# Kernel tuning notes

Measured on AMD Instinct MI355X. Metric: run time of the kernel, lower is better.

Reference implementation:

```python
import jax, jax.numpy as jnp
import numpy as np

N_NODES = 8192
N_UND = 65536      # undirected pairs placed
N_DIR = 131072     # extra directed edges placed


def _build_graph():
    rng = np.random.default_rng(0)
    A = np.zeros((N_NODES, N_NODES), np.float32)
    # undirected pairs (i<j), both directions set
    ii = rng.integers(0, N_NODES, 4 * N_UND)
    jj = rng.integers(0, N_NODES, 4 * N_UND)
    m = ii < jj
    iu, ju = ii[m][:N_UND], jj[m][:N_UND]
    A[iu, ju] = 1.0
    A[ju, iu] = 1.0
    # extra directed edges
    di = rng.integers(0, N_NODES, 2 * N_DIR)
    dj = rng.integers(0, N_NODES, 2 * N_DIR)
    m2 = di != dj
    A[di[m2][:N_DIR], dj[m2][:N_DIR]] = 1.0
    # dense_to_sparse: row, col of nonzeros
    row, col = np.nonzero(A)
    edge_index = np.stack([row, col]).astype(np.int32)
    # undirected mask: A==1 & A.T==1, upper triangle
    und = np.triu((A == 1.0) & (A.T == 1.0))
    u, v = np.nonzero(und)
    undirected_edges = np.stack([u, v], axis=1).astype(np.int32)
    return A, edge_index, undirected_edges


def setup_inputs() -> dict:
    key = jax.random.key(0)
    ks = jax.random.split(key, 4)
    A, edge_index, undirected_edges = _build_graph()
    N = N_NODES
    return {
        "adjacency": jnp.asarray(A),
        "W1": jax.random.normal(ks[0], (N, 16), jnp.float32) * 0.05,
        "b1": jnp.zeros((16,), jnp.float32),
        "W2": jax.random.normal(ks[1], (16, 8), jnp.float32) * 0.25,
        "b2": jnp.zeros((8,), jnp.float32),
        "Wfc": jax.random.normal(ks[2], (16, 1), jnp.float32) * 0.25,
        "bfc": jnp.zeros((1,), jnp.float32),
        "edge_index": jnp.asarray(edge_index),
        "undirected_edges": jnp.asarray(undirected_edges),
    }


def reference(adjacency, W1, b1, W2, b2, Wfc, bfc, edge_index, undirected_edges):
    N = adjacency.shape[0]
    src, dst = edge_index[0], edge_index[1]
    E = src.shape[0]
    # GCN normalization with self-loops (PyG gcn_norm): deg over target nodes
    deg = jax.ops.segment_sum(jnp.ones((E,), adjacency.dtype), dst,
                              num_segments=N) + 1.0
    dinv = jax.lax.rsqrt(deg)                       # deg >= 1, no inf
    norm = dinv[src] * dinv[dst]                    # [E]
    self_w = (dinv * dinv)[:, None]                 # self-loop coeff [N,1]

    def conv(h):  # h: [N, F] -> normalized scatter-add aggregation
        msg = norm[:, None] * h[src]                # [E, F]
        return jax.ops.segment_sum(msg, dst, num_segments=N) + self_w * h

    # node_features = eye(N), so eye(N) @ W1 == W1
    x = jax.nn.relu(conv(W1) + b1)                  # [N, 16]
    x = jax.nn.relu(conv(x @ W2) + b2)              # [N, 8]

    u, v = undirected_edges[:, 0], undirected_edges[:, 1]
    ef = jnp.concatenate([x[u], x[v]], axis=1)      # [U, 16]
    orient = jax.nn.sigmoid(ef @ Wfc + bfc)[:, 0]   # [U]

    out = adjacency.at[u, v].set(orient).at[v, u].set(1.0 - orient)
    return out
```

## Files before the change

kernel.cpp:

```cpp
#include <hip/hip_runtime.h>
#include <math.h>

#define F1 16
#define F2 8

typedef float f32x4 __attribute__((ext_vector_type(4)));

__global__ void k_zero4(f32x4* __restrict__ p, long n4) {
    long i = (long)blockIdx.x * blockDim.x + threadIdx.x;
    long stride = (long)gridDim.x * blockDim.x;
    f32x4 z = {0.0f, 0.0f, 0.0f, 0.0f};
    for (; i < n4; i += stride) {
        __builtin_nontemporal_store(z, &p[i]);
    }
}

__global__ void k_edges0(const int* __restrict__ src, const int* __restrict__ dst,
                         float* __restrict__ out, float* __restrict__ deg,
                         int E, int N) {
    int e = blockIdx.x * blockDim.x + threadIdx.x;
    if (e < E) {
        int s = src[e], d = dst[e];
        out[(long)s * N + d] = 1.0f;
        atomicAdd(&deg[d], 1.0f);
    }
}

__global__ void k_conv1_edges(const int* __restrict__ src, const int* __restrict__ dst,
                              const float* __restrict__ deg, const float* __restrict__ W1,
                              float* __restrict__ x1, int E) {
    int id = blockIdx.x * blockDim.x + threadIdx.x;
    int e = id >> 4;
    int f = id & (F1 - 1);
    if (e < E) {
        int s = src[e], d = dst[e];
        float nrm = rsqrtf((deg[s] + 1.0f) * (deg[d] + 1.0f));
        atomicAdd(&x1[(long)d * F1 + f], nrm * W1[(long)s * F1 + f]);
    }
}

__global__ void k_layer1(const float* __restrict__ deg, const float* __restrict__ b1,
                         const float* __restrict__ W1, const float* __restrict__ W2,
                         const float* __restrict__ x1, float* __restrict__ h2, int N) {
    int id = blockIdx.x * blockDim.x + threadIdx.x;
    if (id < N * F2) {
        int i = id >> 3;
        int g = id & (F2 - 1);
        float sw = 1.0f / (deg[i] + 1.0f);
        float acc = 0.0f;
        #pragma unroll
        for (int f = 0; f < F1; ++f) {
            float v = x1[(long)i * F1 + f] + sw * W1[(long)i * F1 + f] + b1[f];
            v = v > 0.0f ? v : 0.0f;
            acc += v * W2[f * F2 + g];
        }
        h2[(long)i * F2 + g] = acc;
    }
}

__global__ void k_conv2_edges(const int* __restrict__ src, const int* __restrict__ dst,
                              const float* __restrict__ deg, const float* __restrict__ h2,
                              float* __restrict__ x2, int E) {
    int id = blockIdx.x * blockDim.x + threadIdx.x;
    int e = id >> 3;
    int g = id & (F2 - 1);
    if (e < E) {
        int s = src[e], d = dst[e];
        float nrm = rsqrtf((deg[s] + 1.0f) * (deg[d] + 1.0f));
        atomicAdd(&x2[(long)d * F2 + g], nrm * h2[(long)s * F2 + g]);
    }
}

__global__ void k_orient(const int2* __restrict__ ue, const float* __restrict__ x2,
                         const float* __restrict__ h2, const float* __restrict__ deg,
                         const float* __restrict__ b2, const float* __restrict__ Wfc,
                         const float* __restrict__ bfc, float* __restrict__ out,
                         int U, int N) {
    int k = blockIdx.x * blockDim.x + threadIdx.x;
    if (k < U) {
        int2 e = ue[k];
        int u = e.x, v = e.y;
        float swu = 1.0f / (deg[u] + 1.0f);
        float swv = 1.0f / (deg[v] + 1.0f);
        float s = bfc[0];
        #pragma unroll
        for (int g = 0; g < F2; ++g) {
            float xu = x2[(long)u * F2 + g] + swu * h2[(long)u * F2 + g] + b2[g];
            float xv = x2[(long)v * F2 + g] + swv * h2[(long)v * F2 + g] + b2[g];
            xu = xu > 0.0f ? xu : 0.0f;
            xv = xv > 0.0f ? xv : 0.0f;
            s += xu * Wfc[g] + xv * Wfc[F2 + g];
        }
        float orient = 1.0f / (1.0f + expf(-s));
        out[(long)u * N + v] = orient;
        out[(long)v * N + u] = 1.0f - orient;
    }
}

extern "C" void kernel_launch(void* const* d_in, const int* in_sizes, int n_in,
                              void* d_out, int out_size, void* d_ws, size_t ws_size,
                              hipStream_t stream) {
    const float* W1  = (const float*)d_in[1];
    const float* b1  = (const float*)d_in[2];
    const float* W2  = (const float*)d_in[3];
    const float* b2  = (const float*)d_in[4];
    const float* Wfc = (const float*)d_in[5];
    const float* bfc = (const float*)d_in[6];
    const int* edge_index = (const int*)d_in[7];
    const int2* und       = (const int2*)d_in[8];

    int N = in_sizes[1] / F1;
    int E = in_sizes[7] / 2;
    int U = in_sizes[8] / 2;
    const int* src = edge_index;
    const int* dst = edge_index + E;

    float* ws  = (float*)d_ws;
    float* deg = ws;
    float* x1  = ws + N;
    float* x2  = x1 + (long)F1 * N;
    float* h2  = x2 + (long)F2 * N;

    const int B = 256;

    {
        long n4 = ((long)N * N) / 4;
        int blocks = 2048;
        k_zero4<<<blocks, B, 0, stream>>>((f32x4*)d_out, n4);
    }
    (void)hipMemsetAsync(d_ws, 0, (size_t)(N + (long)F1 * N + (long)F2 * N) * sizeof(float), stream);

    k_edges0<<<(E + B - 1) / B, B, 0, stream>>>(src, dst, (float*)d_out, deg, E, N);

    {
        long work = (long)E * F1;
        k_conv1_edges<<<(int)((work + B - 1) / B), B, 0, stream>>>(src, dst, deg, W1, x1, E);
    }
    k_layer1<<<(N * F2 + B - 1) / B, B, 0, stream>>>(deg, b1, W1, W2, x1, h2, N);

    {
        long work = (long)E * F2;
        k_conv2_edges<<<(int)((work + B - 1) / B), B, 0, stream>>>(src, dst, deg, h2, x2, E);
    }

    k_orient<<<(U + B - 1) / B, B, 0, stream>>>(und, x2, h2, deg, b2, Wfc, bfc,
                                                (float*)d_out, U, N);
}
```

Baseline: 478.9 us.

## Replace atomic scatter convolutions with CSR gather via degree scan and bucketing

Integer degrees are counted, exclusive-scanned in a single block into row pointers, and sources are bucketed by destination to form a CSR. Both GCN layers then gather per node without float atomics, with the ReLU, bias and the W2 matmul fused into conv1 through shuffles. The separate layer1 kernel and the workspace memset are removed, and orient reads precomputed activations with vector loads. The cost is extra kernels (a serial single-block scan and an atomic bucketing pass) and nondeterministic neighbour order. The 256 MB output zeroing is untouched, and it probably dominates the runtime.

```diff
diff --git a/kernel.cpp b/kernel.cpp
--- a/kernel.cpp
+++ b/kernel.cpp
@@ -6,94 +6,139 @@
 
 typedef float f32x4 __attribute__((ext_vector_type(4)));
 
-__global__ void k_zero4(f32x4* __restrict__ p, long n4) {
+__global__ void k_zero(f32x4* __restrict__ out, long n4, int* __restrict__ degi, int N) {
     long i = (long)blockIdx.x * blockDim.x + threadIdx.x;
     long stride = (long)gridDim.x * blockDim.x;
+    if (i < N) degi[i] = 0;
     f32x4 z = {0.0f, 0.0f, 0.0f, 0.0f};
-    for (; i < n4; i += stride) {
-        __builtin_nontemporal_store(z, &p[i]);
+    for (long j = i; j < n4; j += stride) {
+        __builtin_nontemporal_store(z, &out[j]);
     }
 }
 
 __global__ void k_edges0(const int* __restrict__ src, const int* __restrict__ dst,
-                         float* __restrict__ out, float* __restrict__ deg,
+                         float* __restrict__ out, int* __restrict__ degi,
                          int E, int N) {
     int e = blockIdx.x * blockDim.x + threadIdx.x;
     if (e < E) {
         int s = src[e], d = dst[e];
         out[(long)s * N + d] = 1.0f;
-        atomicAdd(&deg[d], 1.0f);
+        atomicAdd(&degi[d], 1);
     }
 }
 
-__global__ void k_conv1_edges(const int* __restrict__ src, const int* __restrict__ dst,
-                              const float* __restrict__ deg, const float* __restrict__ W1,
-                              float* __restrict__ x1, int E) {
-    int id = blockIdx.x * blockDim.x + threadIdx.x;
-    int e = id >> 4;
-    int f = id & (F1 - 1);
-    if (e < E) {
-        int s = src[e], d = dst[e];
-        float nrm = rsqrtf((deg[s] + 1.0f) * (deg[d] + 1.0f));
-        atomicAdd(&x1[(long)d * F1 + f], nrm * W1[(long)s * F1 + f]);
+__global__ void k_scan(const int* __restrict__ degi, int* __restrict__ rowptr,
+                       int* __restrict__ cursor, float* __restrict__ dinv, int N) {
+    __shared__ int part[1024];
+    int t = threadIdx.x;
+    int items = (N + 1023) >> 10;
+    int base = t * items;
+    int s = 0;
+    for (int k = 0; k < items; ++k) {
+        int idx = base + k;
+        if (idx < N) s += degi[idx];
+    }
+    part[t] = s;
+    __syncthreads();
+    for (int off = 1; off < 1024; off <<= 1) {
+        int v = (t >= off) ? part[t - off] : 0;
+        __syncthreads();
+        part[t] += v;
+        __syncthreads();
+    }
+    int run = (t == 0) ? 0 : part[t - 1];
+    for (int k = 0; k < items; ++k) {
+        int idx = base + k;
+        if (idx < N) {
+            int dg = degi[idx];
+            rowptr[idx] = run;
+            cursor[idx] = run;
+            dinv[idx] = rsqrtf((float)(dg + 1));
+            run += dg;
+        }
     }
 }
 
-__global__ void k_layer1(const float* __restrict__ deg, const float* __restrict__ b1,
-                         const float* __restrict__ W1, const float* __restrict__ W2,
-                         const float* __restrict__ x1, float* __restrict__ h2, int N) {
-    int id = blockIdx.x * blockDim.x + threadIdx.x;
-    if (id < N * F2) {
-        int i = id >> 3;
-        int g = id & (F2 - 1);
-        float sw = 1.0f / (deg[i] + 1.0f);
-        float acc = 0.0f;
-        #pragma unroll
-        for (int f = 0; f < F1; ++f) {
-            float v = x1[(long)i * F1 + f] + sw * W1[(long)i * F1 + f] + b1[f];
-            v = v > 0.0f ? v : 0.0f;
-            acc += v * W2[f * F2 + g];
-        }
-        h2[(long)i * F2 + g] = acc;
+__global__ void k_bucket(const int* __restrict__ src, const int* __restrict__ dst,
+                         int* __restrict__ cursor, int* __restrict__ sby, int E) {
+    int e = blockIdx.x * blockDim.x + threadIdx.x;
+    if (e < E) {
+        int d = dst[e];
+        int pos = atomicAdd(&cursor[d], 1);
+        sby[pos] = src[e];
     }
 }
 
-__global__ void k_conv2_edges(const int* __restrict__ src, const int* __restrict__ dst,
-                              const float* __restrict__ deg, const float* __restrict__ h2,
-                              float* __restrict__ x2, int E) {
-    int id = blockIdx.x * blockDim.x + threadIdx.x;
-    int e = id >> 3;
-    int g = id & (F2 - 1);
-    if (e < E) {
-        int s = src[e], d = dst[e];
-        float nrm = rsqrtf((deg[s] + 1.0f) * (deg[d] + 1.0f));
-        atomicAdd(&x2[(long)d * F2 + g], nrm * h2[(long)s * F2 + g]);
+__global__ void k_conv1(const int* __restrict__ rowptr, const int* __restrict__ degi,
+                        const int* __restrict__ sby, const float* __restrict__ dinv,
+                        const float* __restrict__ W1, const float* __restrict__ b1,
+                        const float* __restrict__ W2, float* __restrict__ h2, int N) {
+    int tid = blockIdx.x * blockDim.x + threadIdx.x;
+    int node = tid >> 4;
+    int f = tid & (F1 - 1);
+    if (node >= N) return;
+    int r0 = rowptr[node];
+    int r1 = r0 + degi[node];
+    float acc = 0.0f;
+    for (int k = r0; k < r1; ++k) {
+        int s = sby[k];
+        acc += dinv[s] * W1[(long)s * F1 + f];
     }
+    float di = dinv[node];
+    float x = di * acc + di * di * W1[(long)node * F1 + f] + b1[f];
+    float rv = x > 0.0f ? x : 0.0f;
+    int lane = threadIdx.x & 63;
+    int gbase = lane & ~(F1 - 1);
+    int g = f & (F2 - 1);
+    float hg = 0.0f;
+    #pragma unroll
+    for (int ff = 0; ff < F1; ++ff) {
+        float rf = __shfl(rv, gbase + ff, 64);
+        hg += rf * W2[ff * F2 + g];
+    }
+    if (f < F2) h2[(long)node * F2 + g] = hg;
 }
 
-__global__ void k_orient(const int2* __restrict__ ue, const float* __restrict__ x2,
-                         const float* __restrict__ h2, const float* __restrict__ deg,
-                         const float* __restrict__ b2, const float* __restrict__ Wfc,
-                         const float* __restrict__ bfc, float* __restrict__ out,
-                         int U, int N) {
+__global__ void k_conv2(const int* __restrict__ rowptr, const int* __restrict__ degi,
+                        const int* __restrict__ sby, const float* __restrict__ dinv,
+                        const float* __restrict__ h2, const float* __restrict__ b2,
+                        float* __restrict__ xf, int N) {
+    int tid = blockIdx.x * blockDim.x + threadIdx.x;
+    int node = tid >> 3;
+    int g = tid & (F2 - 1);
+    if (node >= N) return;
+    int r0 = rowptr[node];
+    int r1 = r0 + degi[node];
+    float acc = 0.0f;
+    for (int k = r0; k < r1; ++k) {
+        int s = sby[k];
+        acc += dinv[s] * h2[(long)s * F2 + g];
+    }
+    float di = dinv[node];
+    float x = di * acc + di * di * h2[(long)node * F2 + g] + b2[g];
+    xf[(long)node * F2 + g] = x > 0.0f ? x : 0.0f;
+}
+
+__global__ void k_orient(const int2* __restrict__ ue, const float* __restrict__ xf,
+                         const float* __restrict__ Wfc, const float* __restrict__ bfc,
+                         float* __restrict__ out, int U, int N) {
     int k = blockIdx.x * blockDim.x + threadIdx.x;
     if (k < U) {
         int2 e = ue[k];
         int u = e.x, v = e.y;
-        float swu = 1.0f / (deg[u] + 1.0f);
-        float swv = 1.0f / (deg[v] + 1.0f);
+        const f32x4* x4 = (const f32x4*)xf;
+        f32x4 ua = x4[(long)u * 2], ub = x4[(long)u * 2 + 1];
+        f32x4 va = x4[(long)v * 2], vb = x4[(long)v * 2 + 1];
+        const f32x4* w4 = (const f32x4*)Wfc;
+        f32x4 wu0 = w4[0], wu1 = w4[1], wv0 = w4[2], wv1 = w4[3];
         float s = bfc[0];
         #pragma unroll
-        for (int g = 0; g < F2; ++g) {
-            float xu = x2[(long)u * F2 + g] + swu * h2[(long)u * F2 + g] + b2[g];
-            float xv = x2[(long)v * F2 + g] + swv * h2[(long)v * F2 + g] + b2[g];
-            xu = xu > 0.0f ? xu : 0.0f;
-            xv = xv > 0.0f ? xv : 0.0f;
-            s += xu * Wfc[g] + xv * Wfc[F2 + g];
+        for (int g = 0; g < 4; ++g) {
+            s += ua[g] * wu0[g] + ub[g] * wu1[g] + va[g] * wv0[g] + vb[g] * wv1[g];
         }
-        float orient = 1.0f / (1.0f + expf(-s));
-        out[(long)u * N + v] = orient;
-        out[(long)v * N + u] = 1.0f - orient;
+        float o = 1.0f / (1.0f + expf(-s));
+        out[(long)u * N + v] = o;
+        out[(long)v * N + u] = 1.0f - o;
     }
 }
 
@@ -115,34 +160,26 @@
     const int* src = edge_index;
     const int* dst = edge_index + E;
 
-    float* ws  = (float*)d_ws;
-    float* deg = ws;
-    float* x1  = ws + N;
-    float* x2  = x1 + (long)F1 * N;
-    float* h2  = x2 + (long)F2 * N;
+    int*   degi   = (int*)d_ws;
+    int*   rowptr = degi + N;
+    int*   cursor = rowptr + N;
+    float* dinv   = (float*)(cursor + N);
+    int*   sby    = (int*)(dinv + N);
+    float* h2     = (float*)(sby + E);
+    float* xf     = h2 + (long)F2 * N;
 
     const int B = 256;
 
     {
         long n4 = ((long)N * N) / 4;
-        int blocks = 2048;
-        k_zero4<<<blocks, B, 0, stream>>>((f32x4*)d_out, n4);
+        k_zero<<<2048, B, 0, stream>>>((f32x4*)d_out, n4, degi, N);
     }
-    (void)hipMemsetAsync(d_ws, 0, (size_t)(N + (long)F1 * N + (long)F2 * N) * sizeof(float), stream);
-
-    k_edges0<<<(E + B - 1) / B, B, 0, stream>>>(src, dst, (float*)d_out, deg, E, N);
-
-    {
-        long work = (long)E * F1;
-        k_conv1_edges<<<(int)((work + B - 1) / B), B, 0, stream>>>(src, dst, deg, W1, x1, E);
-    }
-    k_layer1<<<(N * F2 + B - 1) / B, B, 0, stream>>>(deg, b1, W1, W2, x1, h2, N);
-
-    {
-        long work = (long)E * F2;
-        k_conv2_edges<<<(int)((work + B - 1) / B), B, 0, stream>>>(src, dst, deg, h2, x2, E);
-    }
-
-    k_orient<<<(U + B - 1) / B, B, 0, stream>>>(und, x2, h2, deg, b2, Wfc, bfc,
-                                                (float*)d_out, U, N);
+    k_edges0<<<(E + B - 1) / B, B, 0, stream>>>(src, dst, (float*)d_out, degi, E, N);
+    k_scan<<<1, 1024, 0, stream>>>(degi, rowptr, cursor, dinv, N);
+    k_bucket<<<(E + B - 1) / B, B, 0, stream>>>(src, dst, cursor, sby, E);
+    k_conv1<<<(N * F1 + B - 1) / B, B, 0, stream>>>(rowptr, degi, sby, dinv,
+                                                    W1, b1, W2, h2, N);
+    k_conv2<<<(N * F2 + B - 1) / B, B, 0, stream>>>(rowptr, degi, sby, dinv,
+                                                    h2, b2, xf, N);
+    k_orient<<<(U + B - 1) / B, B, 0, stream>>>(und, xf, Wfc, bfc, (float*)d_out, U, N);
 }
```

Result: slower. 511.0 us (+6.7%).

## Build CSR of edges and write output rows in one zero-fill-plus-scatter pass

Applied to the files above, without the earlier changes.

Replaces the separate full-matrix zero pass, edge scatter, and scattered orientation writes with a CSR representation. Row pointers come from a binary search over the sorted source array, orientations are written into a per-edge value array found by binary search, and one final kernel per row zeroes the row and scatters its values. This removes the random scattered writes into the 256MB output, which now land in rows that were just written. In exchange it adds binary searches and relies on edge_index being sorted by row and then by column. Degree also becomes an integer atomic counter.

```diff
diff --git a/kernel.cpp b/kernel.cpp
--- a/kernel.cpp
+++ b/kernel.cpp
@@ -6,47 +6,45 @@
 
 typedef float f32x4 __attribute__((ext_vector_type(4)));
 
-__global__ void k_zero4(f32x4* __restrict__ p, long n4) {
-    long i = (long)blockIdx.x * blockDim.x + threadIdx.x;
-    long stride = (long)gridDim.x * blockDim.x;
-    f32x4 z = {0.0f, 0.0f, 0.0f, 0.0f};
-    for (; i < n4; i += stride) {
-        __builtin_nontemporal_store(z, &p[i]);
+__global__ void k_prep(const int* __restrict__ src, const int* __restrict__ dst,
+                       int* __restrict__ degi, float* __restrict__ val,
+                       int* __restrict__ rowptr, int E, int N) {
+    int id = blockIdx.x * blockDim.x + threadIdx.x;
+    if (id < E) {
+        atomicAdd(&degi[dst[id]], 1);
+        val[id] = 1.0f;
     }
-}
-
-__global__ void k_edges0(const int* __restrict__ src, const int* __restrict__ dst,
-                         float* __restrict__ out, float* __restrict__ deg,
-                         int E, int N) {
-    int e = blockIdx.x * blockDim.x + threadIdx.x;
-    if (e < E) {
-        int s = src[e], d = dst[e];
-        out[(long)s * N + d] = 1.0f;
-        atomicAdd(&deg[d], 1.0f);
+    if (id <= N) {
+        int lo = 0, hi = E;
+        while (lo < hi) {
+            int mid = (lo + hi) >> 1;
+            if (src[mid] < id) lo = mid + 1; else hi = mid;
+        }
+        rowptr[id] = lo;
     }
 }
 
 __global__ void k_conv1_edges(const int* __restrict__ src, const int* __restrict__ dst,
-                              const float* __restrict__ deg, const float* __restrict__ W1,
+                              const int* __restrict__ degi, const float* __restrict__ W1,
                               float* __restrict__ x1, int E) {
     int id = blockIdx.x * blockDim.x + threadIdx.x;
     int e = id >> 4;
     int f = id & (F1 - 1);
     if (e < E) {
         int s = src[e], d = dst[e];
-        float nrm = rsqrtf((deg[s] + 1.0f) * (deg[d] + 1.0f));
+        float nrm = rsqrtf((float)((degi[s] + 1) * (degi[d] + 1)));
         atomicAdd(&x1[(long)d * F1 + f], nrm * W1[(long)s * F1 + f]);
     }
 }
 
-__global__ void k_layer1(const float* __restrict__ deg, const float* __restrict__ b1,
+__global__ void k_layer1(const int* __restrict__ degi, const float* __restrict__ b1,
                          const float* __restrict__ W1, const float* __restrict__ W2,
                          const float* __restrict__ x1, float* __restrict__ h2, int N) {
     int id = blockIdx.x * blockDim.x + threadIdx.x;
     if (id < N * F2) {
         int i = id >> 3;
         int g = id & (F2 - 1);
-        float sw = 1.0f / (deg[i] + 1.0f);
+        float sw = 1.0f / (float)(degi[i] + 1);
         float acc = 0.0f;
         #pragma unroll
         for (int f = 0; f < F1; ++f) {
@@ -59,42 +57,61 @@
 }
 
 __global__ void k_conv2_edges(const int* __restrict__ src, const int* __restrict__ dst,
-                              const float* __restrict__ deg, const float* __restrict__ h2,
+                              const int* __restrict__ degi, const float* __restrict__ h2,
                               float* __restrict__ x2, int E) {
     int id = blockIdx.x * blockDim.x + threadIdx.x;
     int e = id >> 3;
     int g = id & (F2 - 1);
     if (e < E) {
         int s = src[e], d = dst[e];
-        float nrm = rsqrtf((deg[s] + 1.0f) * (deg[d] + 1.0f));
+        float nrm = rsqrtf((float)((degi[s] + 1) * (degi[d] + 1)));
         atomicAdd(&x2[(long)d * F2 + g], nrm * h2[(long)s * F2 + g]);
     }
 }
 
-__global__ void k_orient(const int2* __restrict__ ue, const float* __restrict__ x2,
-                         const float* __restrict__ h2, const float* __restrict__ deg,
-                         const float* __restrict__ b2, const float* __restrict__ Wfc,
-                         const float* __restrict__ bfc, float* __restrict__ out,
-                         int U, int N) {
+__global__ void k_orient2(const int2* __restrict__ ue, const float* __restrict__ x2,
+                          const float* __restrict__ h2, const int* __restrict__ degi,
+                          const float* __restrict__ b2, const float* __restrict__ Wfc,
+                          const float* __restrict__ bfc, const int* __restrict__ rowptr,
+                          const int* __restrict__ dst, float* __restrict__ val, int U) {
     int k = blockIdx.x * blockDim.x + threadIdx.x;
-    if (k < U) {
-        int2 e = ue[k];
-        int u = e.x, v = e.y;
-        float swu = 1.0f / (deg[u] + 1.0f);
-        float swv = 1.0f / (deg[v] + 1.0f);
-        float s = bfc[0];
-        #pragma unroll
-        for (int g = 0; g < F2; ++g) {
-            float xu = x2[(long)u * F2 + g] + swu * h2[(long)u * F2 + g] + b2[g];
-            float xv = x2[(long)v * F2 + g] + swv * h2[(long)v * F2 + g] + b2[g];
-            xu = xu > 0.0f ? xu : 0.0f;
-            xv = xv > 0.0f ? xv : 0.0f;
-            s += xu * Wfc[g] + xv * Wfc[F2 + g];
-        }
-        float orient = 1.0f / (1.0f + expf(-s));
-        out[(long)u * N + v] = orient;
-        out[(long)v * N + u] = 1.0f - orient;
+    if (k >= U) return;
+    int2 e = ue[k];
+    int u = e.x, v = e.y;
+    float swu = 1.0f / (float)(degi[u] + 1);
+    float swv = 1.0f / (float)(degi[v] + 1);
+    float s = bfc[0];
+    #pragma unroll
+    for (int g = 0; g < F2; ++g) {
+        float xu = x2[(long)u * F2 + g] + swu * h2[(long)u * F2 + g] + b2[g];
+        float xv = x2[(long)v * F2 + g] + swv * h2[(long)v * F2 + g] + b2[g];
+        xu = xu > 0.0f ? xu : 0.0f;
+        xv = xv > 0.0f ? xv : 0.0f;
+        s += xu * Wfc[g] + xv * Wfc[F2 + g];
     }
+    float o = 1.0f / (1.0f + expf(-s));
+    int lo = rowptr[u], hi = rowptr[u + 1];
+    while (lo < hi) { int mid = (lo + hi) >> 1; if (dst[mid] < v) lo = mid + 1; else hi = mid; }
+    if (lo < rowptr[u + 1] && dst[lo] == v) val[lo] = o;
+    lo = rowptr[v]; hi = rowptr[v + 1];
+    while (lo < hi) { int mid = (lo + hi) >> 1; if (dst[mid] < u) lo = mid + 1; else hi = mid; }
+    if (lo < rowptr[v + 1] && dst[lo] == u) val[lo] = 1.0f - o;
+}
+
+__global__ void __launch_bounds__(256) k_writeout(const int* __restrict__ rowptr,
+                                                  const int* __restrict__ dst,
+                                                  const float* __restrict__ val,
+                                                  float* __restrict__ out, int N) {
+    int row = blockIdx.x;
+    int t = threadIdx.x;
+    int n4 = N >> 2;
+    f32x4* out4 = (f32x4*)(out + (long)row * N);
+    f32x4 z = {0.0f, 0.0f, 0.0f, 0.0f};
+    for (int j = t; j < n4; j += 256) out4[j] = z;
+    __syncthreads();
+    int r0 = rowptr[row], r1 = rowptr[row + 1];
+    float* orow = out + (long)row * N;
+    for (int k = r0 + t; k < r1; k += 256) orow[dst[k]] = val[k];
 }
 
 extern "C" void kernel_launch(void* const* d_in, const int* in_sizes, int n_in,
@@ -115,34 +132,31 @@
     const int* src = edge_index;
     const int* dst = edge_index + E;
 
-    float* ws  = (float*)d_ws;
-    float* deg = ws;
-    float* x1  = ws + N;
-    float* x2  = x1 + (long)F1 * N;
-    float* h2  = x2 + (long)F2 * N;
+    int*   degi   = (int*)d_ws;
+    float* x1     = (float*)(degi + N);
+    float* x2     = x1 + (long)F1 * N;
+    float* h2     = x2 + (long)F2 * N;
+    int*   rowptr = (int*)(h2 + (long)F2 * N);
+    float* val    = (float*)(rowptr + N + 1);
 
     const int B = 256;
 
-    {
-        long n4 = ((long)N * N) / 4;
-        int blocks = 2048;
-        k_zero4<<<blocks, B, 0, stream>>>((f32x4*)d_out, n4);
-    }
     (void)hipMemsetAsync(d_ws, 0, (size_t)(N + (long)F1 * N + (long)F2 * N) * sizeof(float), stream);
 
-    k_edges0<<<(E + B - 1) / B, B, 0, stream>>>(src, dst, (float*)d_out, deg, E, N);
-
+    {
+        int work = (E > N + 1) ? E : (N + 1);
+        k_prep<<<(work + B - 1) / B, B, 0, stream>>>(src, dst, degi, val, rowptr, E, N);
+    }
     {
         long work = (long)E * F1;
-        k_conv1_edges<<<(int)((work + B - 1) / B), B, 0, stream>>>(src, dst, deg, W1, x1, E);
+        k_conv1_edges<<<(int)((work + B - 1) / B), B, 0, stream>>>(src, dst, degi, W1, x1, E);
     }
-    k_layer1<<<(N * F2 + B - 1) / B, B, 0, stream>>>(deg, b1, W1, W2, x1, h2, N);
-
+    k_layer1<<<(N * F2 + B - 1) / B, B, 0, stream>>>(degi, b1, W1, W2, x1, h2, N);
     {
         long work = (long)E * F2;
-        k_conv2_edges<<<(int)((work + B - 1) / B), B, 0, stream>>>(src, dst, deg, h2, x2, E);
+        k_conv2_edges<<<(int)((work + B - 1) / B), B, 0, stream>>>(src, dst, degi, h2, x2, E);
     }
-
-    k_orient<<<(U + B - 1) / B, B, 0, stream>>>(und, x2, h2, deg, b2, Wfc, bfc,
-                                                (float*)d_out, U, N);
+    k_orient2<<<(U + B - 1) / B, B, 0, stream>>>(und, x2, h2, degi, b2, Wfc, bfc,
+                                                 rowptr, dst, val, U);
+    k_writeout<<<N, B, 0, stream>>>(rowptr, dst, val, (float*)d_out, N);
 }
```

Result: faster. 452.5 us (-5.5%).
